# Optimization experiments

Hardware: AMD Instinct MI355X
Metric: run time of the kernel (lower is better)

The kernel has to match this reference:

```python
import jax, jax.numpy as jnp
import numpy as np

N = 100000
E = 3200000
C = 40
L_CORR = 10
L_SMOOTH = 10
ALPHA_CORR = 0.979
ALPHA_SMOOTH = 0.756


def setup_inputs() -> dict:
    key = jax.random.key(0)
    k1, k2, k3, k4 = jax.random.split(key, 4)
    y_true = jax.random.randint(k1, (N,), 0, C, dtype=jnp.int32)
    y_soft = jax.random.uniform(k2, (N, C), dtype=jnp.float32)
    y_soft = y_soft / y_soft.sum(axis=1, keepdims=True)
    spread_mask = jax.random.randint(k3, (N,), 0, 2, dtype=jnp.int32).astype(bool)
    edge_index = jax.random.randint(k4, (2, E), 0, N, dtype=jnp.int32)
    return {"y_true": y_true, "y_soft": y_soft, "spread_mask": spread_mask,
            "edge_index": edge_index}


def _gcn_norm(src, dst, n):
    # symmetric normalization D^-1/2 A D^-1/2 from the edge list
    deg = jax.ops.segment_sum(jnp.ones_like(dst, dtype=jnp.float32), dst,
                              num_segments=n)
    dinv = jnp.where(deg > 0, jax.lax.rsqrt(jnp.maximum(deg, 1.0)), 0.0)
    return dinv[src] * dinv[dst]  # [E]


def _label_prop(y0, src, dst, norm, n, alpha, n_layers, post_step):
    # out <- post_step(alpha * A_hat @ out + (1 - alpha) * y0), repeated
    def body(_, out):
        agg = jax.ops.segment_sum(out[src] * norm[:, None], dst,
                                  num_segments=n)  # [N, C]
        return post_step(alpha * agg + (1.0 - alpha) * y0)
    return jax.lax.fori_loop(0, n_layers, body, y0)


def _correct_and_smooth(y_true, y_soft, spread_mask, edge_index):
    src, dst = edge_index[0], edge_index[1]
    norm = _gcn_norm(src, dst, N)
    onehot = jax.nn.one_hot(y_true, C, dtype=y_soft.dtype)  # [N, C]
    m = spread_mask[:, None]

    # ---- correct: propagate masked residual error, autoscale path ----
    error = jnp.where(m, onehot - y_soft, 0.0)
    smoothed_error = _label_prop(error, src, dst, norm, N, ALPHA_CORR,
                                 L_CORR, lambda x: jnp.clip(x, -1.0, 1.0))
    numel = jnp.sum(spread_mask).astype(y_soft.dtype)
    sigma = jnp.sum(jnp.abs(error)) / numel  # error is zero off-mask
    denom = jnp.sum(jnp.abs(smoothed_error), axis=1, keepdims=True)
    scale = sigma / denom  # [N, 1]
    scale = jnp.where(jnp.isinf(scale) | (scale > 1000.0), 1.0, scale)
    y_corr = y_soft + scale * smoothed_error

    # ---- smooth: inject true labels on spread_mask, propagate w/ softmax ----
    y0 = jnp.where(m, onehot, y_corr)
    out = _label_prop(y0, src, dst, norm, N, ALPHA_SMOOTH, L_SMOOTH,
                      lambda x: jax.nn.softmax(x, axis=-1))
    return out


def reference(y_true, y_soft, spread_mask, edge_index):
    return _correct_and_smooth(y_true, y_soft, spread_mask, edge_index)
```

## Files before the change

### kernel.cpp

```cpp
#include <hip/hip_runtime.h>
#include <hip/hip_fp16.h>
#include <math.h>

#define C 40

__global__ void k_detect(const unsigned int* __restrict__ w, int nwords,
                         unsigned int* __restrict__ flags) {
    int i = blockIdx.x * blockDim.x + threadIdx.x;
    unsigned int viol = 0;
    for (; i < nwords; i += gridDim.x * blockDim.x) {
        unsigned int v = w[i];
        if (!(v == 0u || v == 1u)) viol |= 1u;
        if (!(v == 0u || v == 0x3F800000u)) viol |= 2u;
    }
    if (viol) atomicOr(flags, viol);
}

__device__ __forceinline__ bool read_mask(const void* mp, unsigned int fl, int n) {
    if ((fl & 1u) == 0u) return ((const int*)mp)[n] != 0;
    if ((fl & 2u) == 0u) return ((const float*)mp)[n] != 0.0f;
    return ((const unsigned char*)mp)[n] != 0;
}

__global__ void k_deg(const int* __restrict__ dst, int* __restrict__ deg, int E) {
    int i = blockIdx.x * blockDim.x + threadIdx.x;
    if (i < E) atomicAdd(&deg[dst[i]], 1);
}

__global__ void k_dinv(const int* __restrict__ deg, float* __restrict__ dinv, int n) {
    int i = blockIdx.x * blockDim.x + threadIdx.x;
    if (i < n) {
        int d = deg[i];
        dinv[i] = (d > 0) ? rsqrtf((float)d) : 0.0f;
    }
}

__global__ void k_scan1(const int* __restrict__ deg, int* __restrict__ rowptr,
                        int* __restrict__ bsum, int n) {
    __shared__ int sm[256];
    int tid = threadIdx.x;
    int i = blockIdx.x * 256 + tid;
    int v = (i < n) ? deg[i] : 0;
    sm[tid] = v;
    __syncthreads();
#pragma unroll
    for (int o = 1; o < 256; o <<= 1) {
        int t = (tid >= o) ? sm[tid - o] : 0;
        __syncthreads();
        sm[tid] += t;
        __syncthreads();
    }
    if (i <= n) rowptr[i] = sm[tid] - v;
    if (tid == 255) bsum[blockIdx.x] = sm[255];
}

__global__ void k_scan2(int* __restrict__ bsum, int nb) {
    __shared__ int sm[512];
    int tid = threadIdx.x;
    int v = (tid < nb) ? bsum[tid] : 0;
    sm[tid] = v;
    __syncthreads();
    for (int o = 1; o < 512; o <<= 1) {
        int t = (tid >= o) ? sm[tid - o] : 0;
        __syncthreads();
        sm[tid] += t;
        __syncthreads();
    }
    if (tid < nb) bsum[tid] = sm[tid] - v;
}

__global__ void k_scan3(int* __restrict__ rowptr, const int* __restrict__ bsum, int n) {
    int i = blockIdx.x * 256 + threadIdx.x;
    if (i <= n) rowptr[i] += bsum[blockIdx.x];
}

__global__ void k_csr(const int* __restrict__ src, const int* __restrict__ dst,
                      const float* __restrict__ dinv, const int* __restrict__ rowptr,
                      int* __restrict__ fill, int2* __restrict__ pk, int E) {
    int e = blockIdx.x * blockDim.x + threadIdx.x;
    if (e < E) {
        int s = src[e], d = dst[e];
        int pos = rowptr[d] + atomicAdd(&fill[d], 1);
        int2 v = make_int2(s, __float_as_int(dinv[s] * dinv[d]));
        __builtin_nontemporal_store(*(long long*)&v, (long long*)&pk[pos]);
    }
}

__global__ __launch_bounds__(256) void k_error(
    const float4* __restrict__ ys4, const int* __restrict__ y_true,
    const void* __restrict__ maskp, const unsigned int* __restrict__ flags,
    __half2* __restrict__ errh2, float* __restrict__ psig, float* __restrict__ pcnt,
    int nquads) {
    unsigned int fl = *flags;
    float a = 0.f, cnt = 0.f;
    for (int i = blockIdx.x * blockDim.x + threadIdx.x; i < nquads;
         i += gridDim.x * blockDim.x) {
        int node = i / 10;
        int q = i - node * 10;
        float4 e = make_float4(0.f, 0.f, 0.f, 0.f);
        if (read_mask(maskp, fl, node)) {
            int yt = y_true[node];
            float4 ys = ys4[i];
            int c0 = q * 4;
            e.x = ((c0 + 0) == yt ? 1.f : 0.f) - ys.x;
            e.y = ((c0 + 1) == yt ? 1.f : 0.f) - ys.y;
            e.z = ((c0 + 2) == yt ? 1.f : 0.f) - ys.z;
            e.w = ((c0 + 3) == yt ? 1.f : 0.f) - ys.w;
            a += fabsf(e.x) + fabsf(e.y) + fabsf(e.z) + fabsf(e.w);
            if (q == 0) cnt += 1.f;
        }
        errh2[i * 2] = __floats2half2_rn(e.x, e.y);
        errh2[i * 2 + 1] = __floats2half2_rn(e.z, e.w);
    }
    __shared__ float sA[256];
    __shared__ float sB[256];
    int tid = threadIdx.x;
    sA[tid] = a; sB[tid] = cnt;
    __syncthreads();
    for (int o = 128; o; o >>= 1) {
        if (tid < o) { sA[tid] += sA[tid + o]; sB[tid] += sB[tid + o]; }
        __syncthreads();
    }
    if (tid == 0) { psig[blockIdx.x] = sA[0]; pcnt[blockIdx.x] = sB[0]; }
}

__global__ __launch_bounds__(256) void k_reduce(
    const float* __restrict__ psig, const float* __restrict__ pcnt,
    float* __restrict__ s_sig, float* __restrict__ s_cnt, int nb) {
    float a = 0.f, c = 0.f;
    for (int i = threadIdx.x; i < nb; i += 256) { a += psig[i]; c += pcnt[i]; }
    __shared__ float sA[256];
    __shared__ float sB[256];
    int tid = threadIdx.x;
    sA[tid] = a; sB[tid] = c;
    __syncthreads();
    for (int o = 128; o; o >>= 1) {
        if (tid < o) { sA[tid] += sA[tid + o]; sB[tid] += sB[tid + o]; }
        __syncthreads();
    }
    if (tid == 0) { *s_sig = sA[0]; *s_cnt = sB[0]; }
}

#define PKLOAD(U, EE)                                                        \
    _Pragma("unroll") for (int j = 0; j < GRP; ++j) { U[j] = pk8[(EE) + j]; }

#define GATH(XV, U)                                                          \
    _Pragma("unroll") for (int j = 0; j < GRP; ++j) {                        \
        XV[j] = x[(int)(U[j] & 0xffffffffu) * C + gl];                       \
    }

#define FMAG(U, XV)                                                          \
    _Pragma("unroll") for (int j = 0; j < GRP; ++j) {                        \
        acc[j & 3] = fmaf(__int_as_float((int)(U[j] >> 32)),                 \
                          __half2float(XV[j]), acc[j & 3]);                  \
    }

template <int POST, int F32OUT>
__global__ __launch_bounds__(256) void k_prop(
    const int* __restrict__ rowptr, const unsigned long long* __restrict__ pk8,
    const __half* __restrict__ x, const __half* __restrict__ y0,
    void* __restrict__ outv, float alpha, float beta, int n) {
    int wid = (blockIdx.x * blockDim.x + threadIdx.x) >> 6;
    int lane = threadIdx.x & 63;
    if (wid >= n) return;
    int beg = __builtin_amdgcn_readfirstlane(rowptr[wid]);
    int end = __builtin_amdgcn_readfirstlane(rowptr[wid + 1]);
    int gl = (lane < C) ? lane : 0;
    float y0v = __half2float(y0[wid * C + gl]);
    float acc[4] = {0.f, 0.f, 0.f, 0.f};
    int e = beg;
    {
        enum { GRP = 16 };
        for (; e + GRP <= end; e += GRP) {
            unsigned long long u[GRP];
            __half xv[GRP];
            PKLOAD(u, e)
            GATH(xv, u)
            FMAG(u, xv)
        }
    }
    {
        enum { GRP = 8 };
        if (e + GRP <= end) {
            unsigned long long u[GRP];
            __half xv[GRP];
            PKLOAD(u, e)
            GATH(xv, u)
            FMAG(u, xv)
            e += GRP;
        }
    }
    for (; e < end; ++e) {
        unsigned long long u = pk8[e];
        float xv = __half2float(x[(int)(u & 0xffffffffu) * C + gl]);
        acc[0] = fmaf(__int_as_float((int)(u >> 32)), xv, acc[0]);
    }
    float a = (acc[0] + acc[1]) + (acc[2] + acc[3]);
    float v = fmaf(alpha, a, beta * y0v);

    if (POST == 0) {
        if (lane < C) {
            float res = fminf(1.0f, fmaxf(-1.0f, v));
            if (F32OUT) ((float*)outv)[wid * C + lane] = res;
            else        ((__half*)outv)[wid * C + lane] = __float2half(res);
        }
    } else {
        float mx = (lane < C) ? v : -3.0e38f;
#pragma unroll
        for (int o = 32; o; o >>= 1) mx = fmaxf(mx, __shfl_xor(mx, o));
        float ex = (lane < C) ? __expf(v - mx) : 0.0f;
        float s = ex;
#pragma unroll
        for (int o = 32; o; o >>= 1) s += __shfl_xor(s, o);
        if (lane < C) {
            float res = ex / s;
            if (F32OUT) ((float*)outv)[wid * C + lane] = res;
            else        ((__half*)outv)[wid * C + lane] = __float2half(res);
        }
    }
}

__global__ __launch_bounds__(256) void k_scale(
    const __half* __restrict__ sm_err, const float* __restrict__ y_soft,
    const int* __restrict__ y_true, const void* __restrict__ maskp,
    const unsigned int* __restrict__ flags, const float* __restrict__ s_sig,
    const float* __restrict__ s_cnt, __half* __restrict__ y0, int n) {
    int wid = (blockIdx.x * blockDim.x + threadIdx.x) >> 6;
    int lane = threadIdx.x & 63;
    if (wid >= n) return;
    float v = 0.f, a = 0.f;
    if (lane < C) {
        v = __half2float(sm_err[wid * C + lane]);
        a = fabsf(v);
    }
#pragma unroll
    for (int o = 32; o; o >>= 1) a += __shfl_xor(a, o);
    float sigma = (*s_sig) / (*s_cnt);
    float scale = sigma / a;
    if (isinf(scale) || scale > 1000.0f) scale = 1.0f;
    if (lane < C) {
        bool m = read_mask(maskp, *flags, wid);
        float yc = fmaf(scale, v, y_soft[wid * C + lane]);
        y0[wid * C + lane] = __float2half(m ? ((lane == y_true[wid]) ? 1.0f : 0.0f) : yc);
    }
}

extern "C" void kernel_launch(void* const* d_in, const int* in_sizes, int n_in,
                              void* d_out, int out_size, void* d_ws, size_t ws_size,
                              hipStream_t stream) {
    const int* y_true = (const int*)d_in[0];
    const float* y_soft = (const float*)d_in[1];
    const void* maskp = d_in[2];
    const int* ei = (const int*)d_in[3];
    const int n = in_sizes[0];
    const int total = in_sizes[1];
    const int E = in_sizes[3] / 2;
    const int* src = ei;
    const int* dst = ei + E;

    char* ws = (char*)d_ws;
    size_t off = 0;
    auto alloc = [&](size_t bytes) -> char* {
        char* p = ws + off;
        off += (bytes + 63) & ~(size_t)63;
        return p;
    };
    int* deg = (int*)alloc((size_t)n * 4);
    int* fill = (int*)alloc((size_t)n * 4);
    unsigned int* flags = (unsigned int*)alloc(4);
    size_t zero_bytes = off;
    float* s_sig = (float*)alloc(4);
    float* s_cnt = (float*)alloc(4);
    float* psig = (float*)alloc(2048 * 4);
    float* pcnt = (float*)alloc(2048 * 4);
    float* dinv = (float*)alloc((size_t)n * 4);
    int* rowptr = (int*)alloc((size_t)(n + 1) * 4);
    int* bsum = (int*)alloc(4096);
    int2* pk = (int2*)alloc((size_t)E * 8);
    size_t fbytes = (size_t)total * 2 + 256;
    __half* hE = (__half*)alloc(fbytes);
    __half* hY = (__half*)alloc(fbytes);
    __half* hA = (__half*)alloc(fbytes);
    __half* hB = (__half*)alloc(fbytes);
    (void)ws_size;

    hipMemsetAsync(d_ws, 0, zero_bytes, stream);

    k_detect<<<98, 256, 0, stream>>>((const unsigned int*)maskp, n / 4, flags);
    k_deg<<<(E + 255) / 256, 256, 0, stream>>>(dst, deg, E);
    k_dinv<<<(n + 255) / 256, 256, 0, stream>>>(deg, dinv, n);

    int nb1 = (n + 1 + 255) / 256;
    k_scan1<<<nb1, 256, 0, stream>>>(deg, rowptr, bsum, n);
    k_scan2<<<1, 512, 0, stream>>>(bsum, nb1);
    k_scan3<<<nb1, 256, 0, stream>>>(rowptr, bsum, n);
    k_csr<<<(E + 255) / 256, 256, 0, stream>>>(src, dst, dinv, rowptr, fill, pk, E);

    k_error<<<2048, 256, 0, stream>>>((const float4*)y_soft, y_true, maskp, flags,
                                      (__half2*)hE, psig, pcnt, total / 4);
    k_reduce<<<1, 256, 0, stream>>>(psig, pcnt, s_sig, s_cnt, 2048);

    const int pb = (n + 3) / 4;
    const float A1 = 0.979f, B1 = (float)(1.0 - 0.979);
    const float A2 = 0.756f, B2 = (float)(1.0 - 0.756);
    __half* bufs[2] = { hA, hB };
    const unsigned long long* pk8 = (const unsigned long long*)pk;

    const __half* x = hE;
    for (int it = 0; it < 10; ++it) {
        k_prop<0, 0><<<pb, 256, 0, stream>>>(rowptr, pk8, x, hE, bufs[it & 1], A1, B1, n);
        x = bufs[it & 1];
    }
    k_scale<<<pb, 256, 0, stream>>>(x, y_soft, y_true, maskp, flags, s_sig, s_cnt, hY, n);

    x = hY;
    for (int it = 0; it < 9; ++it) {
        k_prop<1, 0><<<pb, 256, 0, stream>>>(rowptr, pk8, x, hY, bufs[it & 1], A2, B2, n);
        x = bufs[it & 1];
    }
    k_prop<1, 1><<<pb, 256, 0, stream>>>(rowptr, pk8, x, hY, d_out, A2, B2, n);
}
```

Measured before the change: 1.590 ms.

## Split fp16 node features into aligned 32-channel and 8-channel planes

```diff
diff --git a/kernel.cpp b/kernel.cpp
--- a/kernel.cpp
+++ b/kernel.cpp
@@ -35,12 +35,12 @@
     }
 }
 
-__global__ void k_scan1(const int* __restrict__ deg, int* __restrict__ rowptr,
+__global__ void k_scan1(const int* __restrict__ in, int* __restrict__ outp,
                         int* __restrict__ bsum, int n) {
     __shared__ int sm[256];
     int tid = threadIdx.x;
     int i = blockIdx.x * 256 + tid;
-    int v = (i < n) ? deg[i] : 0;
+    int v = (i < n) ? in[i] : 0;
     sm[tid] = v;
     __syncthreads();
 #pragma unroll
@@ -50,7 +50,7 @@
         sm[tid] += t;
         __syncthreads();
     }
-    if (i <= n) rowptr[i] = sm[tid] - v;
+    if (i <= n) outp[i] = sm[tid] - v;
     if (tid == 255) bsum[blockIdx.x] = sm[255];
 }
 
@@ -69,48 +69,58 @@
     if (tid < nb) bsum[tid] = sm[tid] - v;
 }
 
-__global__ void k_scan3(int* __restrict__ rowptr, const int* __restrict__ bsum, int n) {
+__global__ void k_scan3(int* __restrict__ outp, const int* __restrict__ bsum, int n) {
     int i = blockIdx.x * 256 + threadIdx.x;
-    if (i <= n) rowptr[i] += bsum[blockIdx.x];
+    if (i <= n) outp[i] += bsum[blockIdx.x];
 }
 
 __global__ void k_csr(const int* __restrict__ src, const int* __restrict__ dst,
                       const float* __restrict__ dinv, const int* __restrict__ rowptr,
-                      int* __restrict__ fill, int2* __restrict__ pk, int E) {
+                      int* __restrict__ fill, unsigned long long* __restrict__ pk,
+                      int E) {
     int e = blockIdx.x * blockDim.x + threadIdx.x;
     if (e < E) {
         int s = src[e], d = dst[e];
         int pos = rowptr[d] + atomicAdd(&fill[d], 1);
-        int2 v = make_int2(s, __float_as_int(dinv[s] * dinv[d]));
-        __builtin_nontemporal_store(*(long long*)&v, (long long*)&pk[pos]);
+        unsigned long long u = (unsigned)s |
+            ((unsigned long long)(unsigned)__float_as_int(dinv[s] * dinv[d]) << 32);
+        pk[pos] = u;
     }
 }
 
 __global__ __launch_bounds__(256) void k_error(
     const float4* __restrict__ ys4, const int* __restrict__ y_true,
     const void* __restrict__ maskp, const unsigned int* __restrict__ flags,
-    __half2* __restrict__ errh2, float* __restrict__ psig, float* __restrict__ pcnt,
-    int nquads) {
+    char* __restrict__ err, float* __restrict__ psig, float* __restrict__ pcnt,
+    int n) {
     unsigned int fl = *flags;
+    unsigned boff = (unsigned)n * 64u;
     float a = 0.f, cnt = 0.f;
-    for (int i = blockIdx.x * blockDim.x + threadIdx.x; i < nquads;
+    int nq = n * 10;
+    for (int i = blockIdx.x * blockDim.x + threadIdx.x; i < nq;
          i += gridDim.x * blockDim.x) {
         int node = i / 10;
         int q = i - node * 10;
-        float4 e = make_float4(0.f, 0.f, 0.f, 0.f);
+        float e0 = 0.f, e1 = 0.f, e2 = 0.f, e3 = 0.f;
         if (read_mask(maskp, fl, node)) {
             int yt = y_true[node];
             float4 ys = ys4[i];
             int c0 = q * 4;
-            e.x = ((c0 + 0) == yt ? 1.f : 0.f) - ys.x;
-            e.y = ((c0 + 1) == yt ? 1.f : 0.f) - ys.y;
-            e.z = ((c0 + 2) == yt ? 1.f : 0.f) - ys.z;
-            e.w = ((c0 + 3) == yt ? 1.f : 0.f) - ys.w;
-            a += fabsf(e.x) + fabsf(e.y) + fabsf(e.z) + fabsf(e.w);
+            e0 = ((c0 + 0) == yt ? 1.f : 0.f) - ys.x;
+            e1 = ((c0 + 1) == yt ? 1.f : 0.f) - ys.y;
+            e2 = ((c0 + 2) == yt ? 1.f : 0.f) - ys.z;
+            e3 = ((c0 + 3) == yt ? 1.f : 0.f) - ys.w;
+            a += fabsf(e0) + fabsf(e1) + fabsf(e2) + fabsf(e3);
             if (q == 0) cnt += 1.f;
         }
-        errh2[i * 2] = __floats2half2_rn(e.x, e.y);
-        errh2[i * 2 + 1] = __floats2half2_rn(e.z, e.w);
+        __half2 h01 = __floats2half2_rn(e0, e1);
+        __half2 h23 = __floats2half2_rn(e2, e3);
+        uint2 w;
+        w.x = *(unsigned*)&h01;
+        w.y = *(unsigned*)&h23;
+        unsigned off = (q < 8) ? (unsigned)node * 64u + (unsigned)q * 8u
+                               : boff + (unsigned)node * 16u + (unsigned)(q - 8) * 8u;
+        *(uint2*)(err + off) = w;
     }
     __shared__ float sA[256];
     __shared__ float sB[256];
@@ -146,7 +156,8 @@
 
 #define GATH(XV, U)                                                          \
     _Pragma("unroll") for (int j = 0; j < GRP; ++j) {                        \
-        XV[j] = x[(int)(U[j] & 0xffffffffu) * C + gl];                       \
+        unsigned s = (unsigned)(U[j] & 0xffffffffu);                         \
+        XV[j] = *(const __half*)(xc + ((s << shift) + aoff));                \
     }
 
 #define FMAG(U, XV)                                                          \
@@ -158,15 +169,19 @@
 template <int POST, int F32OUT>
 __global__ __launch_bounds__(256) void k_prop(
     const int* __restrict__ rowptr, const unsigned long long* __restrict__ pk8,
-    const __half* __restrict__ x, const __half* __restrict__ y0,
+    const char* __restrict__ xc, const char* __restrict__ y0,
     void* __restrict__ outv, float alpha, float beta, int n) {
     int wid = (blockIdx.x * blockDim.x + threadIdx.x) >> 6;
     int lane = threadIdx.x & 63;
     if (wid >= n) return;
     int beg = __builtin_amdgcn_readfirstlane(rowptr[wid]);
     int end = __builtin_amdgcn_readfirstlane(rowptr[wid + 1]);
-    int gl = (lane < C) ? lane : 0;
-    float y0v = __half2float(y0[wid * C + gl]);
+    bool isA = (lane < 32);
+    unsigned shift = isA ? 6u : 4u;
+    unsigned aoff = isA ? (unsigned)(lane * 2)
+                        : (unsigned)n * 64u + (unsigned)((lane - 32) * 2);
+
+    float y0v = __half2float(*(const __half*)(y0 + (((unsigned)wid << shift) + aoff)));
     float acc[4] = {0.f, 0.f, 0.f, 0.f};
     int e = beg;
     {
@@ -192,18 +207,16 @@
     }
     for (; e < end; ++e) {
         unsigned long long u = pk8[e];
-        float xv = __half2float(x[(int)(u & 0xffffffffu) * C + gl]);
+        unsigned s = (unsigned)(u & 0xffffffffu);
+        float xv = __half2float(*(const __half*)(xc + ((s << shift) + aoff)));
         acc[0] = fmaf(__int_as_float((int)(u >> 32)), xv, acc[0]);
     }
     float a = (acc[0] + acc[1]) + (acc[2] + acc[3]);
     float v = fmaf(alpha, a, beta * y0v);
 
+    float res;
     if (POST == 0) {
-        if (lane < C) {
-            float res = fminf(1.0f, fmaxf(-1.0f, v));
-            if (F32OUT) ((float*)outv)[wid * C + lane] = res;
-            else        ((__half*)outv)[wid * C + lane] = __float2half(res);
-        }
+        res = fminf(1.0f, fmaxf(-1.0f, v));
     } else {
         float mx = (lane < C) ? v : -3.0e38f;
 #pragma unroll
@@ -212,25 +225,33 @@
         float s = ex;
 #pragma unroll
         for (int o = 32; o; o >>= 1) s += __shfl_xor(s, o);
-        if (lane < C) {
-            float res = ex / s;
-            if (F32OUT) ((float*)outv)[wid * C + lane] = res;
-            else        ((__half*)outv)[wid * C + lane] = __float2half(res);
+        res = ex / s;
+    }
+    if (lane < C) {
+        if (F32OUT) {
+            ((float*)outv)[(size_t)wid * C + lane] = res;
+        } else {
+            *(__half*)((char*)outv + (((unsigned)wid << shift) + aoff)) =
+                __float2half(res);
         }
     }
 }
 
 __global__ __launch_bounds__(256) void k_scale(
-    const __half* __restrict__ sm_err, const float* __restrict__ y_soft,
+    const char* __restrict__ sm_err, const float* __restrict__ y_soft,
     const int* __restrict__ y_true, const void* __restrict__ maskp,
     const unsigned int* __restrict__ flags, const float* __restrict__ s_sig,
-    const float* __restrict__ s_cnt, __half* __restrict__ y0, int n) {
+    const float* __restrict__ s_cnt, char* __restrict__ y0, int n) {
     int wid = (blockIdx.x * blockDim.x + threadIdx.x) >> 6;
     int lane = threadIdx.x & 63;
     if (wid >= n) return;
+    bool isA = (lane < 32);
+    unsigned shift = isA ? 6u : 4u;
+    unsigned aoff = isA ? (unsigned)(lane * 2)
+                        : (unsigned)n * 64u + (unsigned)((lane - 32) * 2);
     float v = 0.f, a = 0.f;
     if (lane < C) {
-        v = __half2float(sm_err[wid * C + lane]);
+        v = __half2float(*(const __half*)(sm_err + (((unsigned)wid << shift) + aoff)));
         a = fabsf(v);
     }
 #pragma unroll
@@ -240,8 +261,9 @@
     if (isinf(scale) || scale > 1000.0f) scale = 1.0f;
     if (lane < C) {
         bool m = read_mask(maskp, *flags, wid);
-        float yc = fmaf(scale, v, y_soft[wid * C + lane]);
-        y0[wid * C + lane] = __float2half(m ? ((lane == y_true[wid]) ? 1.0f : 0.0f) : yc);
+        float yc = fmaf(scale, v, y_soft[(size_t)wid * C + lane]);
+        float r = m ? ((lane == y_true[wid]) ? 1.0f : 0.0f) : yc;
+        *(__half*)(y0 + (((unsigned)wid << shift) + aoff)) = __float2half(r);
     }
 }
 
@@ -253,7 +275,6 @@
     const void* maskp = d_in[2];
     const int* ei = (const int*)d_in[3];
     const int n = in_sizes[0];
-    const int total = in_sizes[1];
     const int E = in_sizes[3] / 2;
     const int* src = ei;
     const int* dst = ei + E;
@@ -262,7 +283,7 @@
     size_t off = 0;
     auto alloc = [&](size_t bytes) -> char* {
         char* p = ws + off;
-        off += (bytes + 63) & ~(size_t)63;
+        off += (bytes + 255) & ~(size_t)255;
         return p;
     };
     int* deg = (int*)alloc((size_t)n * 4);
@@ -276,12 +297,12 @@
     float* dinv = (float*)alloc((size_t)n * 4);
     int* rowptr = (int*)alloc((size_t)(n + 1) * 4);
     int* bsum = (int*)alloc(4096);
-    int2* pk = (int2*)alloc((size_t)E * 8);
-    size_t fbytes = (size_t)total * 2 + 256;
-    __half* hE = (__half*)alloc(fbytes);
-    __half* hY = (__half*)alloc(fbytes);
-    __half* hA = (__half*)alloc(fbytes);
-    __half* hB = (__half*)alloc(fbytes);
+    unsigned long long* pk = (unsigned long long*)alloc((size_t)E * 8);
+    size_t fb = (size_t)n * 80 + 512;
+    char* hE = alloc(fb);
+    char* hY = alloc(fb);
+    char* hA = alloc(fb);
+    char* hB = alloc(fb);
     (void)ws_size;
 
     hipMemsetAsync(d_ws, 0, zero_bytes, stream);
@@ -297,26 +318,25 @@
     k_csr<<<(E + 255) / 256, 256, 0, stream>>>(src, dst, dinv, rowptr, fill, pk, E);
 
     k_error<<<2048, 256, 0, stream>>>((const float4*)y_soft, y_true, maskp, flags,
-                                      (__half2*)hE, psig, pcnt, total / 4);
+                                      hE, psig, pcnt, n);
     k_reduce<<<1, 256, 0, stream>>>(psig, pcnt, s_sig, s_cnt, 2048);
 
     const int pb = (n + 3) / 4;
     const float A1 = 0.979f, B1 = (float)(1.0 - 0.979);
     const float A2 = 0.756f, B2 = (float)(1.0 - 0.756);
-    __half* bufs[2] = { hA, hB };
-    const unsigned long long* pk8 = (const unsigned long long*)pk;
-
-    const __half* x = hE;
+    char* bufs[2] = { hA, hB };
+
+    const char* x = hE;
     for (int it = 0; it < 10; ++it) {
-        k_prop<0, 0><<<pb, 256, 0, stream>>>(rowptr, pk8, x, hE, bufs[it & 1], A1, B1, n);
+        k_prop<0, 0><<<pb, 256, 0, stream>>>(rowptr, pk, x, hE, bufs[it & 1], A1, B1, n);
         x = bufs[it & 1];
     }
     k_scale<<<pb, 256, 0, stream>>>(x, y_soft, y_true, maskp, flags, s_sig, s_cnt, hY, n);
 
     x = hY;
     for (int it = 0; it < 9; ++it) {
-        k_prop<1, 0><<<pb, 256, 0, stream>>>(rowptr, pk8, x, hY, bufs[it & 1], A2, B2, n);
+        k_prop<1, 0><<<pb, 256, 0, stream>>>(rowptr, pk, x, hY, bufs[it & 1], A2, B2, n);
         x = bufs[it & 1];
     }
-    k_prop<1, 1><<<pb, 256, 0, stream>>>(rowptr, pk8, x, hY, d_out, A2, B2, n);
-}
+    k_prop<1, 1><<<pb, 256, 0, stream>>>(rowptr, pk, x, hY, d_out, A2, B2, n);
+}
```

Measured after the change: 1.602 ms. About the same (+0.7%).
